# Kernel optimization log

Hardware: AMD Instinct MI355X
Metric: run time of the kernel (lower is better)

The kernel has to match this reference:

```python
import jax, jax.numpy as jnp
import numpy as np

K = 8  # number of nearest color neighbors
P = 2  # l2 mode


def setup_inputs() -> dict:
    key = jax.random.key(0)
    k1, k2 = jax.random.split(key)
    predictions = jax.random.uniform(k1, (4, 128, 8), dtype=jnp.float32)
    ref_imgs = jax.random.uniform(k2, (4, 3, 256, 256), dtype=jnp.float32)
    return {"predictions": predictions, "ref_imgs": ref_imgs}


def reference(predictions, ref_imgs):
    bs, L, _ = predictions.shape
    ch = ref_imgs.shape[1]
    img_size = ref_imgs.shape[-1]
    preds_position = predictions[:, :, :2]  # (bs, L, 2) normalized (x, y)

    # --- grid_sample(nearest, border, align_corners=False) color lookup ---
    # Original code flattens the grid bs-major ((i//L, i%L)) but tiles images
    # L-major (image index i % bs); we replicate that exact pairing.
    grid_flat = jax.lax.stop_gradient(preds_position).reshape(bs * L, 2)
    # unnormalize: x_pix = g * size - 0.5, then nearest + border clamp
    ix = jnp.clip(jnp.round(grid_flat[:, 0] * img_size - 0.5), 0, img_size - 1).astype(jnp.int32)
    iy = jnp.clip(jnp.round(grid_flat[:, 1] * img_size - 0.5), 0, img_size - 1).astype(jnp.int32)
    b_img = jnp.arange(bs * L, dtype=jnp.int32) % bs
    pooled_flat = ref_imgs[b_img, :, iy, ix]  # (bs*L, ch)
    # original rearrange '(L bs) ch 1 1 -> bs L ch 1 1': out[b,l] = flat[l*bs+b]
    pooled = pooled_flat.reshape(L, bs, ch).transpose(1, 0, 2)  # (bs, L, ch)

    # --- dense color-similarity map over the whole image ---
    sim = jnp.mean(jnp.abs(ref_imgs[:, None] - pooled[:, :, :, None, None]), axis=2)  # (bs, L, H, W)

    # --- topK best-matching pixel locations ---
    _, idx = jax.lax.top_k(-sim.reshape(bs, L, img_size * img_size), K)  # (bs, L, K)
    inv_size = jnp.float32(1.0 / img_size)
    tgt_y = (idx // img_size).astype(jnp.float32) * inv_size
    tgt_x = (idx % img_size).astype(jnp.float32) * inv_size
    tgt = jnp.stack([tgt_x, tgt_y], axis=-1)  # (bs, L, K, 2)
    tgt_down = jnp.roll(tgt, shift=1, axis=1)

    # --- min distance to previous stroke's candidate positions ---
    # cdist rows are identical (pred position repeated K times), so the
    # min over the last dim reduces to a single (bs, L, K) distance.
    diff = preds_position[:, :, None, :] - tgt_down  # (bs, L, K, 2)
    if P == 2:
        dist = jnp.sqrt(jnp.sum(diff * diff, axis=-1))
    else:
        dist = jnp.sum(jnp.abs(diff), axis=-1)
    val_down = jnp.min(dist, axis=-1)  # (bs, L)
    loss = jnp.mean(val_down[:, 1:])
    return loss
```

## Files before the change

### kernel.cpp

```cpp
#include <hip/hip_runtime.h>
#include <math.h>

#define BS 4
#define LQ 128
#define IMG 256
#define NPIX (IMG*IMG)
#define NSLICE 4
#define SLICE_PIX (NPIX/NSLICE)
#define SLICE_F4  (SLICE_PIX/4)
#define CAP 512

__device__ __forceinline__ bool lessVI(float v1, int i1, float v2, int i2) {
    return (v1 < v2) || (v1 == v2 && i1 < i2);
}

#define CE8(WV, WI, a, c)                                                     \
    do {                                                                      \
        if (lessVI((WV)[c], (WI)[c], (WV)[a], (WI)[a])) {                     \
            float tv_ = (WV)[a]; (WV)[a] = (WV)[c]; (WV)[c] = tv_;            \
            int   ti_ = (WI)[a]; (WI)[a] = (WI)[c]; (WI)[c] = ti_;            \
        }                                                                     \
    } while (0)

#define MERGE8(AV, AI, BV, BI, OV, OI)                                        \
    do {                                                                      \
        _Pragma("unroll")                                                     \
        for (int k_ = 0; k_ < 8; ++k_) {                                      \
            if (lessVI((AV)[k_], (AI)[k_], (BV)[7-k_], (BI)[7-k_])) {         \
                (OV)[k_] = (AV)[k_]; (OI)[k_] = (AI)[k_];                     \
            } else { (OV)[k_] = (BV)[7-k_]; (OI)[k_] = (BI)[7-k_]; }          \
        }                                                                     \
        CE8(OV, OI, 0, 4); CE8(OV, OI, 1, 5); CE8(OV, OI, 2, 6); CE8(OV, OI, 3, 7); \
        CE8(OV, OI, 0, 2); CE8(OV, OI, 1, 3); CE8(OV, OI, 4, 6); CE8(OV, OI, 5, 7); \
        CE8(OV, OI, 0, 1); CE8(OV, OI, 2, 3); CE8(OV, OI, 4, 5); CE8(OV, OI, 6, 7); \
    } while (0)

__global__ __launch_bounds__(512)
void scan_kernel(const float* __restrict__ pred,
                 const float* __restrict__ imgs,
                 float* __restrict__ wsv,
                 int* __restrict__ wsi) {
    __shared__ float pool[2][3];
    __shared__ float ltau[2];
    __shared__ int   cnt[2];
    __shared__ float swv[8][8];
    __shared__ float lv[2][CAP];
    __shared__ int   li[2][CAP];

    const int bid = blockIdx.x;
    const int b  = (bid & 7) >> 1;
    const int u  = bid >> 3;
    const int sl = u & (NSLICE - 1);
    const int qp = (u >> 2) | ((bid & 1) << 5);
    const int tid  = threadIdx.x;
    const int qsel = tid >> 8;
    const int st   = tid & 255;
    const int l    = qp * 2 + qsel;

    const int n  = l * BS + b;
    const int pb = n >> 7;
    const int pl = n & (LQ - 1);
    const float px = pred[(pb * LQ + pl) * 8 + 0];
    const float py = pred[(pb * LQ + pl) * 8 + 1];
    const int ix = (int)fminf(fmaxf(rintf(px * 256.0f - 0.5f), 0.0f), 255.0f);
    const int iy = (int)fminf(fmaxf(rintf(py * 256.0f - 0.5f), 0.0f), 255.0f);
    const float* img = imgs + b * 3 * NPIX;
    const int pc = iy * IMG + ix;
    const float c0 = img[pc];
    const float c1 = img[NPIX + pc];
    const float c2 = img[2 * NPIX + pc];
    if (st == 0) {
        pool[qsel][0] = c0; pool[qsel][1] = c1; pool[qsel][2] = c2;
    }
    if (tid < 2) cnt[tid] = 0;

    float tb[8];
#pragma unroll
    for (int k = 0; k < 8; ++k) tb[k] = 3.0e38f;
#pragma unroll 4
    for (int j = 0; j < 16; ++j) {
        const int p = sl * SLICE_PIX + j * 1024 + st;
        const float a0 = img[p];
        const float a1 = img[NPIX + p];
        const float a2 = img[2 * NPIX + p];
        const float s = fabsf(a0 - c0) + fabsf(a1 - c1) + fabsf(a2 - c2);
        if (s < tb[7]) {
            tb[7] = s;
#pragma unroll
            for (int k = 7; k > 0; --k) {
                if (tb[k] < tb[k - 1]) { float t = tb[k]; tb[k] = tb[k - 1]; tb[k - 1] = t; }
            }
        }
    }
#pragma unroll
    for (int off = 1; off < 64; off <<= 1) {
        float ov[8];
#pragma unroll
        for (int k = 0; k < 8; ++k) ov[k] = __shfl_xor(tb[k], off, 64);
        float w[8];
#pragma unroll
        for (int k = 0; k < 8; ++k) w[k] = fminf(tb[k], ov[7 - k]);
#define CEV(a, c) do { float lo = fminf(w[a], w[c]); float hi = fmaxf(w[a], w[c]); w[a] = lo; w[c] = hi; } while (0)
        CEV(0, 4); CEV(1, 5); CEV(2, 6); CEV(3, 7);
        CEV(0, 2); CEV(1, 3); CEV(4, 6); CEV(5, 7);
        CEV(0, 1); CEV(2, 3); CEV(4, 5); CEV(6, 7);
#undef CEV
#pragma unroll
        for (int k = 0; k < 8; ++k) tb[k] = w[k];
    }
    const int wid  = tid >> 6;
    const int lane = tid & 63;
    if (lane == 0) {
#pragma unroll
        for (int k = 0; k < 8; ++k) swv[wid][k] = tb[k];
    }
    __syncthreads();
    if ((tid & 255) == 0) {
        const int q = tid >> 8;
        const int base = q * 4;
        int ptr[4] = {0, 0, 0, 0};
        float last = 0.0f;
        for (int r = 0; r < 8; ++r) {
            int best = 0; float bvv = swv[base][ptr[0]];
            for (int w = 1; w < 4; ++w) {
                float vv = swv[base + w][ptr[w]];
                if (vv < bvv) { best = w; bvv = vv; }
            }
            last = bvv;
            ptr[best]++;
        }
        ltau[q] = last;
    }
    __syncthreads();

    const float t0 = ltau[0], t1 = ltau[1];
    const float q00 = pool[0][0], q01 = pool[0][1], q02 = pool[0][2];
    const float q10 = pool[1][0], q11 = pool[1][1], q12 = pool[1][2];
    const float4* i0 = (const float4*)img;
    const float4* i1 = (const float4*)(img + NPIX);
    const float4* i2 = (const float4*)(img + 2 * NPIX);

    const int base4 = sl * SLICE_F4;
#pragma unroll 2
    for (int it = 0; it < SLICE_F4 / 512; ++it) {
        const int q4 = base4 + it * 512 + tid;
        const float4 a0 = i0[q4];
        const float4 a1 = i1[q4];
        const float4 a2 = i2[q4];
        const int p = q4 * 4;
#define PROC(vx, vy, vz, pix)                                                  \
        do {                                                                   \
            const float s0 = fabsf((vx) - q00) + fabsf((vy) - q01) + fabsf((vz) - q02); \
            if (s0 <= t0) {                                                    \
                const int pos = atomicAdd(&cnt[0], 1);                         \
                if (pos < CAP) { lv[0][pos] = s0; li[0][pos] = (pix); }        \
            }                                                                  \
            const float s1 = fabsf((vx) - q10) + fabsf((vy) - q11) + fabsf((vz) - q12); \
            if (s1 <= t1) {                                                    \
                const int pos = atomicAdd(&cnt[1], 1);                         \
                if (pos < CAP) { lv[1][pos] = s1; li[1][pos] = (pix); }        \
            }                                                                  \
        } while (0)
        PROC(a0.x, a1.x, a2.x, p + 0);
        PROC(a0.y, a1.y, a2.y, p + 1);
        PROC(a0.z, a1.z, a2.z, p + 2);
        PROC(a0.w, a1.w, a2.w, p + 3);
#undef PROC
    }
    __syncthreads();

    if ((wid & 3) == 0) {
        const int q = wid >> 2;
        const int nels = min(cnt[q], CAP);
        float bv[8]; int bi[8];
#pragma unroll
        for (int k = 0; k < 8; ++k) { bv[k] = 3.0e38f; bi[k] = 0x7FFFFFFF; }
        for (int c = lane; c < nels; c += 64) {
            const float v = lv[q][c];
            const int  id = li[q][c];
            if (lessVI(v, id, bv[7], bi[7])) {
                bv[7] = v; bi[7] = id;
#pragma unroll
                for (int k = 7; k > 0; --k) {
                    if (lessVI(bv[k], bi[k], bv[k - 1], bi[k - 1])) {
                        float tv = bv[k]; bv[k] = bv[k - 1]; bv[k - 1] = tv;
                        int   ti = bi[k]; bi[k] = bi[k - 1]; bi[k - 1] = ti;
                    }
                }
            }
        }
#pragma unroll
        for (int off = 1; off < 64; off <<= 1) {
            float ov[8]; int oi[8];
#pragma unroll
            for (int k = 0; k < 8; ++k) {
                ov[k] = __shfl_xor(bv[k], off, 64);
                oi[k] = __shfl_xor(bi[k], off, 64);
            }
            float w[8]; int wi[8];
#pragma unroll
            for (int k = 0; k < 8; ++k) {
                if (lessVI(bv[k], bi[k], ov[7 - k], oi[7 - k])) { w[k] = bv[k];     wi[k] = bi[k]; }
                else                                            { w[k] = ov[7 - k]; wi[k] = oi[7 - k]; }
            }
            CE8(w, wi, 0, 4); CE8(w, wi, 1, 5); CE8(w, wi, 2, 6); CE8(w, wi, 3, 7);
            CE8(w, wi, 0, 2); CE8(w, wi, 1, 3); CE8(w, wi, 4, 6); CE8(w, wi, 5, 7);
            CE8(w, wi, 0, 1); CE8(w, wi, 2, 3); CE8(w, wi, 4, 5); CE8(w, wi, 6, 7);
#pragma unroll
            for (int k = 0; k < 8; ++k) { bv[k] = w[k]; bi[k] = wi[k]; }
        }
        if (lane == 0) {
            const int mq = b * LQ + qp * 2 + q;
            const int slot = mq * (NSLICE * 8) + sl * 8;
#pragma unroll
            for (int k = 0; k < 8; ++k) { wsv[slot + k] = bv[k]; wsi[slot + k] = bi[k]; }
        }
    }
}

__global__ __launch_bounds__(512)
void loss_kernel(const float* __restrict__ pred,
                 const float* __restrict__ wsv,
                 const int* __restrict__ wsi,
                 float* __restrict__ out) {
    __shared__ float red[512];
    const int t = threadIdx.x;
    const int b = t >> 7;
    const int l = t & (LQ - 1);
    float v = 0.0f;
    if (l >= 1) {
        const int mq = b * LQ + (l - 1);
        float av[4][8]; int ai[4][8];
#pragma unroll
        for (int s = 0; s < 4; ++s) {
#pragma unroll
            for (int k = 0; k < 8; ++k) {
                av[s][k] = wsv[mq * 32 + s * 8 + k];
                ai[s][k] = wsi[mq * 32 + s * 8 + k];
            }
        }
        float m0v[8]; int m0i[8];
        float m1v[8]; int m1i[8];
        float fv[8];  int fi[8];
        MERGE8(av[0], ai[0], av[1], ai[1], m0v, m0i);
        MERGE8(av[2], ai[2], av[3], ai[3], m1v, m1i);
        MERGE8(m0v, m0i, m1v, m1i, fv, fi);

        const float px = pred[(b * LQ + l) * 8 + 0];
        const float py = pred[(b * LQ + l) * 8 + 1];
        float best = 3.0e38f;
#pragma unroll
        for (int k = 0; k < 8; ++k) {
            const int id = fi[k];
            const float tx = (float)(id & (IMG - 1)) * (1.0f / IMG);
            const float ty = (float)(id >> 8)        * (1.0f / IMG);
            const float dx = px - tx;
            const float dy = py - ty;
            best = fminf(best, sqrtf(dx * dx + dy * dy));
        }
        v = best;
    }
    red[t] = v;
    __syncthreads();
    for (int s = 256; s > 0; s >>= 1) {
        if (t < s) red[t] += red[t + s];
        __syncthreads();
    }
    if (t == 0) out[0] = red[0] * (1.0f / (BS * (LQ - 1)));
}

extern "C" void kernel_launch(void* const* d_in, const int* in_sizes, int n_in,
                              void* d_out, int out_size, void* d_ws, size_t ws_size,
                              hipStream_t stream) {
    const float* pred = (const float*)d_in[0];
    const float* imgs = (const float*)d_in[1];
    float* out = (float*)d_out;
    float* wsv = (float*)d_ws;
    int*   wsi = (int*)((char*)d_ws + 512 * 32 * sizeof(float));

    hipLaunchKernelGGL(scan_kernel, dim3(BS * 64 * NSLICE), dim3(512), 0, stream,
                       pred, imgs, wsv, wsi);
    hipLaunchKernelGGL(loss_kernel, dim3(1), dim3(512), 0, stream,
                       pred, wsv, wsi, out);
}
```

Baseline: 41.76 us.

## Fuse scan and loss kernels with histogram threshold and last-block reduction

Replaces the per-thread sorted top-8 threshold estimation with a shared-memory histogram over a sample of pixels that picks a conservative bin cutoff. Each block now handles 4 queries over 8 slices instead of 2 queries over 4 slices, so each loaded pixel is reused across more queries. The separate loss kernel is folded in: the last block to finish, found through an atomic counter, merges the slice candidates and computes the loss. A memset is added for the counter. The histogram threshold can admit many candidates and overflow CAP, which risks both correctness and atomic contention.

```diff
diff --git a/kernel.cpp b/kernel.cpp
--- a/kernel.cpp
+++ b/kernel.cpp
@@ -5,10 +5,14 @@
 #define LQ 128
 #define IMG 256
 #define NPIX (IMG*IMG)
-#define NSLICE 4
+#define NQ 4
+#define NSLICE 8
 #define SLICE_PIX (NPIX/NSLICE)
-#define SLICE_F4  (SLICE_PIX/4)
+#define SLICE_F4 (SLICE_PIX/4)
+#define NBINS 128
 #define CAP 512
+#define NBLK (BS*(LQ/NQ)*NSLICE)
+#define SCALE (128.0f/3.0f)
 
 __device__ __forceinline__ bool lessVI(float v1, int i1, float v2, int i2) {
     return (v1 < v2) || (v1 == v2 && i1 < i2);
@@ -36,146 +40,115 @@
     } while (0)
 
 __global__ __launch_bounds__(512)
-void scan_kernel(const float* __restrict__ pred,
-                 const float* __restrict__ imgs,
-                 float* __restrict__ wsv,
-                 int* __restrict__ wsi) {
-    __shared__ float pool[2][3];
-    __shared__ float ltau[2];
-    __shared__ int   cnt[2];
-    __shared__ float swv[8][8];
-    __shared__ float lv[2][CAP];
-    __shared__ int   li[2][CAP];
+void fused_kernel(const float* __restrict__ pred,
+                  const float* __restrict__ imgs,
+                  float2* __restrict__ ws,
+                  int* __restrict__ counter,
+                  float* __restrict__ out) {
+    __shared__ float pool[NQ][3];
+    __shared__ int   hist[NQ][NBINS];
+    __shared__ int   Bq[NQ];
+    __shared__ int   cnt[NQ];
+    __shared__ float lv[NQ][CAP];
+    __shared__ int   li[NQ][CAP];
+    __shared__ float mv[NQ][2][8];
+    __shared__ int   mi[NQ][2][8];
+    __shared__ int   lastflag;
+    __shared__ float red[512];
 
     const int bid = blockIdx.x;
     const int b  = (bid & 7) >> 1;
     const int u  = bid >> 3;
     const int sl = u & (NSLICE - 1);
-    const int qp = (u >> 2) | ((bid & 1) << 5);
-    const int tid  = threadIdx.x;
-    const int qsel = tid >> 8;
-    const int st   = tid & 255;
-    const int l    = qp * 2 + qsel;
-
+    const int qg = (u >> 3) | ((bid & 1) << 4);
+    const int tid = threadIdx.x;
+    const int qi = tid >> 7;
+    const int st = tid & 127;
+
+    ((int*)hist)[tid] = 0;
+    if (tid < NQ) cnt[tid] = 0;
+
+    const int l  = qg * NQ + qi;
     const int n  = l * BS + b;
     const int pb = n >> 7;
     const int pl = n & (LQ - 1);
-    const float px = pred[(pb * LQ + pl) * 8 + 0];
-    const float py = pred[(pb * LQ + pl) * 8 + 1];
-    const int ix = (int)fminf(fmaxf(rintf(px * 256.0f - 0.5f), 0.0f), 255.0f);
-    const int iy = (int)fminf(fmaxf(rintf(py * 256.0f - 0.5f), 0.0f), 255.0f);
+    const float gx = pred[(pb * LQ + pl) * 8 + 0];
+    const float gy = pred[(pb * LQ + pl) * 8 + 1];
+    const int ix = (int)fminf(fmaxf(rintf(gx * 256.0f - 0.5f), 0.0f), 255.0f);
+    const int iy = (int)fminf(fmaxf(rintf(gy * 256.0f - 0.5f), 0.0f), 255.0f);
     const float* img = imgs + b * 3 * NPIX;
     const int pc = iy * IMG + ix;
     const float c0 = img[pc];
     const float c1 = img[NPIX + pc];
     const float c2 = img[2 * NPIX + pc];
-    if (st == 0) {
-        pool[qsel][0] = c0; pool[qsel][1] = c1; pool[qsel][2] = c2;
-    }
-    if (tid < 2) cnt[tid] = 0;
-
-    float tb[8];
-#pragma unroll
-    for (int k = 0; k < 8; ++k) tb[k] = 3.0e38f;
-#pragma unroll 4
-    for (int j = 0; j < 16; ++j) {
+    if (st == 0) { pool[qi][0] = c0; pool[qi][1] = c1; pool[qi][2] = c2; }
+    __syncthreads();
+
+#pragma unroll
+    for (int j = 0; j < 8; ++j) {
         const int p = sl * SLICE_PIX + j * 1024 + st;
-        const float a0 = img[p];
-        const float a1 = img[NPIX + p];
-        const float a2 = img[2 * NPIX + p];
-        const float s = fabsf(a0 - c0) + fabsf(a1 - c1) + fabsf(a2 - c2);
-        if (s < tb[7]) {
-            tb[7] = s;
-#pragma unroll
-            for (int k = 7; k > 0; --k) {
-                if (tb[k] < tb[k - 1]) { float t = tb[k]; tb[k] = tb[k - 1]; tb[k - 1] = t; }
-            }
-        }
-    }
-#pragma unroll
-    for (int off = 1; off < 64; off <<= 1) {
-        float ov[8];
-#pragma unroll
-        for (int k = 0; k < 8; ++k) ov[k] = __shfl_xor(tb[k], off, 64);
-        float w[8];
-#pragma unroll
-        for (int k = 0; k < 8; ++k) w[k] = fminf(tb[k], ov[7 - k]);
-#define CEV(a, c) do { float lo = fminf(w[a], w[c]); float hi = fmaxf(w[a], w[c]); w[a] = lo; w[c] = hi; } while (0)
-        CEV(0, 4); CEV(1, 5); CEV(2, 6); CEV(3, 7);
-        CEV(0, 2); CEV(1, 3); CEV(4, 6); CEV(5, 7);
-        CEV(0, 1); CEV(2, 3); CEV(4, 5); CEV(6, 7);
-#undef CEV
-#pragma unroll
-        for (int k = 0; k < 8; ++k) tb[k] = w[k];
-    }
-    const int wid  = tid >> 6;
-    const int lane = tid & 63;
-    if (lane == 0) {
-#pragma unroll
-        for (int k = 0; k < 8; ++k) swv[wid][k] = tb[k];
-    }
-    __syncthreads();
-    if ((tid & 255) == 0) {
-        const int q = tid >> 8;
-        const int base = q * 4;
-        int ptr[4] = {0, 0, 0, 0};
-        float last = 0.0f;
-        for (int r = 0; r < 8; ++r) {
-            int best = 0; float bvv = swv[base][ptr[0]];
-            for (int w = 1; w < 4; ++w) {
-                float vv = swv[base + w][ptr[w]];
-                if (vv < bvv) { best = w; bvv = vv; }
-            }
-            last = bvv;
-            ptr[best]++;
-        }
-        ltau[q] = last;
-    }
-    __syncthreads();
-
-    const float t0 = ltau[0], t1 = ltau[1];
-    const float q00 = pool[0][0], q01 = pool[0][1], q02 = pool[0][2];
-    const float q10 = pool[1][0], q11 = pool[1][1], q12 = pool[1][2];
+        const float s = fabsf(img[p] - c0) + fabsf(img[NPIX + p] - c1)
+                      + fabsf(img[2 * NPIX + p] - c2);
+        int bn = (int)(s * SCALE);
+        bn = bn > (NBINS - 1) ? (NBINS - 1) : bn;
+        atomicAdd(&hist[qi][bn], 1);
+    }
+    __syncthreads();
+    if (tid < NQ) {
+        int cum = 0, bn = 0;
+        while (bn < NBINS && cum < 8) { cum += hist[tid][bn]; ++bn; }
+        Bq[tid] = bn - 1;
+    }
+    __syncthreads();
+
+    float P0[NQ], P1[NQ], P2[NQ], T[NQ];
+#pragma unroll
+    for (int q = 0; q < NQ; ++q) {
+        P0[q] = pool[q][0]; P1[q] = pool[q][1]; P2[q] = pool[q][2];
+        const int B = Bq[q];
+        T[q] = (B >= NBINS - 1) ? 3.0e38f : (float)(B + 1);
+    }
+
     const float4* i0 = (const float4*)img;
     const float4* i1 = (const float4*)(img + NPIX);
     const float4* i2 = (const float4*)(img + 2 * NPIX);
-
-    const int base4 = sl * SLICE_F4;
-#pragma unroll 2
+#pragma unroll
     for (int it = 0; it < SLICE_F4 / 512; ++it) {
-        const int q4 = base4 + it * 512 + tid;
+        const int q4 = sl * SLICE_F4 + it * 512 + tid;
         const float4 a0 = i0[q4];
         const float4 a1 = i1[q4];
         const float4 a2 = i2[q4];
         const int p = q4 * 4;
-#define PROC(vx, vy, vz, pix)                                                  \
-        do {                                                                   \
-            const float s0 = fabsf((vx) - q00) + fabsf((vy) - q01) + fabsf((vz) - q02); \
-            if (s0 <= t0) {                                                    \
-                const int pos = atomicAdd(&cnt[0], 1);                         \
-                if (pos < CAP) { lv[0][pos] = s0; li[0][pos] = (pix); }        \
-            }                                                                  \
-            const float s1 = fabsf((vx) - q10) + fabsf((vy) - q11) + fabsf((vz) - q12); \
-            if (s1 <= t1) {                                                    \
-                const int pos = atomicAdd(&cnt[1], 1);                         \
-                if (pos < CAP) { lv[1][pos] = s1; li[1][pos] = (pix); }        \
-            }                                                                  \
+#define PX(vx, vy, vz, pp)                                                    \
+        do {                                                                  \
+            _Pragma("unroll")                                                 \
+            for (int q = 0; q < NQ; ++q) {                                    \
+                const float s = fabsf((vx) - P0[q]) + fabsf((vy) - P1[q])     \
+                              + fabsf((vz) - P2[q]);                          \
+                if (s * SCALE < T[q]) {                                       \
+                    const int pos = atomicAdd(&cnt[q], 1);                    \
+                    if (pos < CAP) { lv[q][pos] = s; li[q][pos] = (pp); }     \
+                }                                                             \
+            }                                                                 \
         } while (0)
-        PROC(a0.x, a1.x, a2.x, p + 0);
-        PROC(a0.y, a1.y, a2.y, p + 1);
-        PROC(a0.z, a1.z, a2.z, p + 2);
-        PROC(a0.w, a1.w, a2.w, p + 3);
-#undef PROC
-    }
-    __syncthreads();
-
-    if ((wid & 3) == 0) {
-        const int q = wid >> 2;
+        PX(a0.x, a1.x, a2.x, p + 0);
+        PX(a0.y, a1.y, a2.y, p + 1);
+        PX(a0.z, a1.z, a2.z, p + 2);
+        PX(a0.w, a1.w, a2.w, p + 3);
+#undef PX
+    }
+    __syncthreads();
+
+    const int wid  = tid >> 6;
+    const int lane = tid & 63;
+    {
+        const int q    = wid >> 1;
+        const int half = wid & 1;
         const int nels = min(cnt[q], CAP);
         float bv[8]; int bi[8];
 #pragma unroll
         for (int k = 0; k < 8; ++k) { bv[k] = 3.0e38f; bi[k] = 0x7FFFFFFF; }
-        for (int c = lane; c < nels; c += 64) {
+        for (int c = half * 64 + lane; c < nels; c += 128) {
             const float v = lv[q][c];
             const int  id = li[q][c];
             if (lessVI(v, id, bv[7], bi[7])) {
@@ -210,63 +183,86 @@
             for (int k = 0; k < 8; ++k) { bv[k] = w[k]; bi[k] = wi[k]; }
         }
         if (lane == 0) {
-            const int mq = b * LQ + qp * 2 + q;
-            const int slot = mq * (NSLICE * 8) + sl * 8;
-#pragma unroll
-            for (int k = 0; k < 8; ++k) { wsv[slot + k] = bv[k]; wsi[slot + k] = bi[k]; }
-        }
-    }
-}
-
-__global__ __launch_bounds__(512)
-void loss_kernel(const float* __restrict__ pred,
-                 const float* __restrict__ wsv,
-                 const int* __restrict__ wsi,
-                 float* __restrict__ out) {
-    __shared__ float red[512];
-    const int t = threadIdx.x;
-    const int b = t >> 7;
-    const int l = t & (LQ - 1);
-    float v = 0.0f;
-    if (l >= 1) {
-        const int mq = b * LQ + (l - 1);
-        float av[4][8]; int ai[4][8];
-#pragma unroll
-        for (int s = 0; s < 4; ++s) {
-#pragma unroll
-            for (int k = 0; k < 8; ++k) {
-                av[s][k] = wsv[mq * 32 + s * 8 + k];
-                ai[s][k] = wsi[mq * 32 + s * 8 + k];
-            }
-        }
-        float m0v[8]; int m0i[8];
-        float m1v[8]; int m1i[8];
-        float fv[8];  int fi[8];
-        MERGE8(av[0], ai[0], av[1], ai[1], m0v, m0i);
-        MERGE8(av[2], ai[2], av[3], ai[3], m1v, m1i);
-        MERGE8(m0v, m0i, m1v, m1i, fv, fi);
-
-        const float px = pred[(b * LQ + l) * 8 + 0];
-        const float py = pred[(b * LQ + l) * 8 + 1];
-        float best = 3.0e38f;
+#pragma unroll
+            for (int k = 0; k < 8; ++k) { mv[q][half][k] = bv[k]; mi[q][half][k] = bi[k]; }
+        }
+    }
+    __syncthreads();
+
+    if (st == 0) {
+        float av[8], bv2[8], ov[8]; int ai[8], bi2[8], oi[8];
 #pragma unroll
         for (int k = 0; k < 8; ++k) {
-            const int id = fi[k];
-            const float tx = (float)(id & (IMG - 1)) * (1.0f / IMG);
-            const float ty = (float)(id >> 8)        * (1.0f / IMG);
-            const float dx = px - tx;
-            const float dy = py - ty;
-            best = fminf(best, sqrtf(dx * dx + dy * dy));
-        }
-        v = best;
-    }
-    red[t] = v;
-    __syncthreads();
-    for (int s = 256; s > 0; s >>= 1) {
-        if (t < s) red[t] += red[t + s];
+            av[k] = mv[qi][0][k]; ai[k] = mi[qi][0][k];
+            bv2[k] = mv[qi][1][k]; bi2[k] = mi[qi][1][k];
+        }
+        MERGE8(av, ai, bv2, bi2, ov, oi);
+        const int mq = b * LQ + qg * NQ + qi;
+        float2* o = ws + (mq * NSLICE + sl) * 8;
+#pragma unroll
+        for (int k = 0; k < 8; ++k) {
+            float2 e; e.x = ov[k]; e.y = __int_as_float(oi[k]);
+            o[k] = e;
+        }
+    }
+    __syncthreads();
+
+    if (tid == 0) {
+        __threadfence();
+        const int t = atomicAdd(counter, 1);
+        lastflag = ((t % NBLK) == (NBLK - 1)) ? 1 : 0;
+    }
+    __syncthreads();
+    if (!lastflag) return;
+    __threadfence();
+
+    {
+        const int b2 = tid >> 7;
+        const int l2 = tid & (LQ - 1);
+        float v = 0.0f;
+        if (l2 >= 1) {
+            const int mq = b2 * LQ + (l2 - 1);
+            const float2* base = ws + mq * (NSLICE * 8);
+            float fv[8]; int fi[8];
+#pragma unroll
+            for (int k = 0; k < 8; ++k) {
+                const float2 e = base[k];
+                fv[k] = e.x; fi[k] = __float_as_int(e.y);
+            }
+#pragma unroll
+            for (int s2 = 1; s2 < NSLICE; ++s2) {
+                float av[8], ov[8]; int ai[8], oi[8];
+#pragma unroll
+                for (int k = 0; k < 8; ++k) {
+                    const float2 e = base[s2 * 8 + k];
+                    av[k] = e.x; ai[k] = __float_as_int(e.y);
+                }
+                MERGE8(fv, fi, av, ai, ov, oi);
+#pragma unroll
+                for (int k = 0; k < 8; ++k) { fv[k] = ov[k]; fi[k] = oi[k]; }
+            }
+            const float qx = pred[(b2 * LQ + l2) * 8 + 0];
+            const float qy = pred[(b2 * LQ + l2) * 8 + 1];
+            float best = 3.0e38f;
+#pragma unroll
+            for (int k = 0; k < 8; ++k) {
+                const int id = fi[k];
+                const float tx = (float)(id & (IMG - 1)) * (1.0f / IMG);
+                const float ty = (float)(id >> 8)        * (1.0f / IMG);
+                const float dx = qx - tx;
+                const float dy = qy - ty;
+                best = fminf(best, sqrtf(dx * dx + dy * dy));
+            }
+            v = best;
+        }
+        red[tid] = v;
         __syncthreads();
-    }
-    if (t == 0) out[0] = red[0] * (1.0f / (BS * (LQ - 1)));
+        for (int s = 256; s > 0; s >>= 1) {
+            if (tid < s) red[tid] += red[tid + s];
+            __syncthreads();
+        }
+        if (tid == 0) out[0] = red[0] * (1.0f / (BS * (LQ - 1)));
+    }
 }
 
 extern "C" void kernel_launch(void* const* d_in, const int* in_sizes, int n_in,
@@ -275,11 +271,10 @@
     const float* pred = (const float*)d_in[0];
     const float* imgs = (const float*)d_in[1];
     float* out = (float*)d_out;
-    float* wsv = (float*)d_ws;
-    int*   wsi = (int*)((char*)d_ws + 512 * 32 * sizeof(float));
-
-    hipLaunchKernelGGL(scan_kernel, dim3(BS * 64 * NSLICE), dim3(512), 0, stream,
-                       pred, imgs, wsv, wsi);
-    hipLaunchKernelGGL(loss_kernel, dim3(1), dim3(512), 0, stream,
-                       pred, wsv, wsi, out);
+    int* counter = (int*)d_ws;
+    float2* ws = (float2*)((char*)d_ws + 256);
+
+    hipMemsetAsync(counter, 0, 4, stream);
+    hipLaunchKernelGGL(fused_kernel, dim3(NBLK), dim3(512), 0, stream,
+                       pred, imgs, ws, counter, out);
 }
```

Measured after the change: 62.72 us. +50.2%, slower.
